# Performance work log

Measured on AMD Instinct MI355X. Metric: run time of the kernel, lower is better.

Reference implementation:

```python
import jax, jax.numpy as jnp
import numpy as np

SIM_RATIO = 0.5
TAU = 1e-4


def _gumbel_softmax_hard(logits, u, axis=-1):
    # torch F.gumbel_softmax(hard=True): straight-through one-hot
    eps = 1e-7
    g = -jnp.log(-jnp.log(u * (1.0 - 2.0 * eps) + eps))
    y_soft = jax.nn.softmax((logits + g) / TAU, axis=axis)
    idx = jnp.argmax(y_soft, axis=axis)
    y_hard = jax.nn.one_hot(idx, logits.shape[axis], dtype=y_soft.dtype)
    return y_hard - jax.lax.stop_gradient(y_soft) + y_soft


def setup_inputs() -> dict:
    key = jax.random.key(0)
    ks = jax.random.split(key, 7)
    N, S, n_items, n_users, d = 4096, 500, 100000, 50000, 64
    need_replace = jax.random.randint(ks[0], (N, 2), 0, n_users)  # user<n_users, item<n_users<=n_items ok
    union_feature = jax.random.normal(ks[1], (N, 2 * d), dtype=jnp.float32)
    all_items = jax.random.normal(ks[2], (n_items, d), dtype=jnp.float32)
    sample_items = jax.random.randint(ks[3], (n_users, S), 0, n_items)
    W = jax.random.normal(ks[4], (d, 2 * d), dtype=jnp.float32) * (1.0 / np.sqrt(2 * d))
    b = jax.random.normal(ks[5], (d,), dtype=jnp.float32) * 0.01
    gumbel_u = jax.random.uniform(ks[6], (N, S), dtype=jnp.float32)
    return {"need_replace": need_replace, "union_feature": union_feature,
            "all_items": all_items, "sample_items": sample_items,
            "W": W, "b": b, "gumbel_u": gumbel_u}


def reference(need_replace, union_feature, all_items, sample_items, W, b, gumbel_u):
    S = sample_items.shape[1]
    user_ids = need_replace[:, 0]
    item_ids = need_replace[:, 1]

    items_emb = all_items[item_ids][:, None, :]          # [N,1,d]
    samp = sample_items[user_ids]                        # [N,S]
    samp_feat = all_items[samp]                          # [N,S,d]

    rank_score = jnp.sum(items_emb * samp_feat, axis=-1)         # [N,S]
    item_ranking = jnp.argsort(rank_score, axis=1)               # ascending sort indices
    item_reverse = jnp.argsort(item_ranking, axis=1)             # rank of each candidate
    sample_item_sort = jnp.take_along_axis(samp, item_ranking, axis=1)  # [N,S]

    uif = union_feature @ W.T + b                                # [N,d]
    replace_score = jnp.sum(uif[:, None, :] * samp_feat, axis=-1)  # [N,S]

    rp = _gumbel_softmax_hard(replace_score, gumbel_u)           # [N,S] one-hot (ST)

    position_index = jnp.sum(item_reverse.astype(rp.dtype) * rp, axis=-1) + 1.0
    similarity = position_index / S
    # MarginLoss (assumed): mean absolute deviation from target ratio
    similarity_loss = jnp.mean(jnp.abs(similarity - SIM_RATIO))

    replaceable_items = jnp.sum(sample_item_sort.astype(rp.dtype) * rp, axis=-1).astype(jnp.int32)
    replaceable_items_feature = jnp.sum(samp_feat * rp[:, :, None], axis=1)  # [N,d]

    return replaceable_items, replaceable_items_feature, similarity_loss, jnp.mean(similarity)
```

## Files before the change

kernel.cpp:

```cpp
#include <hip/hip_runtime.h>

#define SDIM 500
#define DDIM 64
#define NT   256

__device__ __forceinline__ unsigned ford(float x) {
    unsigned u = __float_as_uint(x);
    return u ^ ((unsigned)((int)u >> 31) | 0x80000000u);
}

__device__ __forceinline__ float dot16(float4 a0, float4 a1, float4 a2, float4 a3,
                                       float4 b0, float4 b1, float4 b2, float4 b3) {
    return a0.x*b0.x + a0.y*b0.y + a0.z*b0.z + a0.w*b0.w
         + a1.x*b1.x + a1.y*b1.y + a1.z*b1.z + a1.w*b1.w
         + a2.x*b2.x + a2.y*b2.y + a2.z*b2.z + a2.w*b2.w
         + a3.x*b3.x + a3.y*b3.y + a3.z*b3.z + a3.w*b3.w;
}

__global__ __launch_bounds__(NT) void rs_main(
    const int* __restrict__ need_replace,
    const float* __restrict__ union_feature,
    const float* __restrict__ all_items,
    const int* __restrict__ sample_items,
    const float* __restrict__ Wm,
    const float* __restrict__ bv,
    const float* __restrict__ gumbel_u,
    float* __restrict__ out_items,
    float* __restrict__ out_feat,
    float* __restrict__ ws_sim)
{
    __shared__ __align__(16) float s_uf[128];
    __shared__ __align__(16) float s_uif[DDIM];
    __shared__ unsigned s_fv[SDIM];
    __shared__ float    s_key[SDIM];
    __shared__ int      s_samp[SDIM];
    __shared__ int      s_hist[256];
    __shared__ float    s_mv[4];
    __shared__ int      s_mi[4];
    __shared__ int      s_cnt4[4];
    __shared__ int      s_selb, s_selk, s_k, s_tn;
    __shared__ int      s_tbuf[64];

    const int n    = blockIdx.x;
    const int tid  = threadIdx.x;
    const int wid  = tid >> 6;
    const int part = tid & 3, quad = tid >> 2;

    const int user = need_replace[2 * n];
    const int item = need_replace[2 * n + 1];
    const int*   samp_row = sample_items + (long)user * SDIM;
    const float* gur      = gumbel_u + (long)n * SDIM;

    if (tid < 128) s_uf[tid] = union_feature[(long)n * 128 + tid];
    for (int s = tid; s < SDIM; s += NT) s_samp[s] = samp_row[s];
    const float4* ir = (const float4*)(all_items + (long)item * DDIM) + part * 4;
    const float4 wiA = ir[0], wiB = ir[1], wiC = ir[2], wiD = ir[3];
    __syncthreads();

    {
        const float4* wr4 = (const float4*)(Wm + (long)quad * 128);
        const float4* uf4 = (const float4*)s_uf;
        float acc = 0.f;
        #pragma unroll
        for (int q = 0; q < 8; ++q) {
            float4 w4 = wr4[part + q * 4];
            float4 u4 = uf4[part + q * 4];
            acc += w4.x * u4.x + w4.y * u4.y + w4.z * u4.z + w4.w * u4.w;
        }
        acc += __shfl_xor(acc, 1);
        acc += __shfl_xor(acc, 2);
        if (part == 0) s_uif[quad] = acc + bv[quad];
    }
    __syncthreads();
    const float4* ur = (const float4*)s_uif + part * 4;
    const float4 wuA = ur[0], wuB = ur[1], wuC = ur[2], wuD = ur[3];

    float4 f0, f1, f2, f3;
    {
        const float4* p = (const float4*)(all_items + (long)s_samp[quad] * DDIM) + part * 4;
        f0 = p[0]; f1 = p[1]; f2 = p[2]; f3 = p[3];
    }
    #pragma unroll
    for (int i = 0; i < 8; ++i) {
        const int s = i * 64 + quad;
        float4 g0 = f0, g1 = f1, g2 = f2, g3 = f3;
        if (i < 7) {
            const int sn = s + 64;
            const bool actn = (sn < SDIM);
            const int idxn = s_samp[actn ? sn : 0];
            const float4* q = (const float4*)(all_items + (long)idxn * DDIM) + part * 4;
            if (actn) { g0 = q[0]; g1 = q[1]; g2 = q[2]; g3 = q[3]; }
        }
        const bool act = (s < SDIM);
        float a0 = dot16(f0, f1, f2, f3, wiA, wiB, wiC, wiD);
        float a1 = dot16(f0, f1, f2, f3, wuA, wuB, wuC, wuD);
        a0 += __shfl_xor(a0, 1); a0 += __shfl_xor(a0, 2);
        a1 += __shfl_xor(a1, 1); a1 += __shfl_xor(a1, 2);
        if (act && part == 0) { s_fv[s] = ford(a0); s_key[s] = a1; }
        f0 = g0; f1 = g1; f2 = g2; f3 = g3;
    }
    __syncthreads();

    {
        float bvv = -__builtin_inff();
        int   bii = SDIM;
        for (int s = tid; s < SDIM; s += NT) {
            float u = gur[s];
            float g = -logf(-logf(u * (1.0f - 2e-7f) + 1e-7f));
            float v = s_key[s] + g;
            if (v > bvv) { bvv = v; bii = s; }
        }
        #pragma unroll
        for (int off = 1; off < 64; off <<= 1) {
            float v2 = __shfl_xor(bvv, off); int i2 = __shfl_xor(bii, off);
            if (v2 > bvv || (v2 == bvv && i2 < bii)) { bvv = v2; bii = i2; }
        }
        if ((tid & 63) == 0) { s_mv[wid] = bvv; s_mi[wid] = bii; }
        __syncthreads();
        if (tid == 0) {
            float mv = s_mv[0]; int mi = s_mi[0];
            #pragma unroll
            for (int w = 1; w < 4; ++w) {
                float v2 = s_mv[w]; int i2 = s_mi[w];
                if (v2 > mv || (v2 == mv && i2 < mi)) { mv = v2; mi = i2; }
            }
            s_k = mi;
        }
        __syncthreads();
    }
    const int k = s_k;

    {
        const int src = s_samp[k];
        if (tid < DDIM)
            out_feat[(long)n * DDIM + tid] = all_items[(long)src * DDIM + tid];
    }

    int rank_k;
    {
        const unsigned fvk = s_fv[k];
        int cnt = 0;
        for (int s = tid; s < SDIM; s += NT) {
            unsigned v = s_fv[s];
            cnt += (int)((v < fvk) | ((v == fvk) & (s < k)));
        }
        #pragma unroll
        for (int off = 1; off < 64; off <<= 1) cnt += __shfl_xor(cnt, off);
        if ((tid & 63) == 0) s_cnt4[wid] = cnt;
        __syncthreads();
        rank_k = s_cnt4[0] + s_cnt4[1] + s_cnt4[2] + s_cnt4[3];
    }

    unsigned prefix = 0;
    int krem = k;
    for (int pass = 0; pass < 4; ++pass) {
        const int shift = 24 - 8 * pass;
        s_hist[tid] = 0;
        __syncthreads();
        const unsigned himask = pass ? (0xFFFFFFFFu << (shift + 8)) : 0u;
        for (int s = tid; s < SDIM; s += NT) {
            unsigned v = s_fv[s];
            if ((v & himask) == prefix) atomicAdd(&s_hist[(v >> shift) & 0xFF], 1);
        }
        __syncthreads();
        if (tid < 64) {
            int h0 = s_hist[4*tid], h1 = s_hist[4*tid+1], h2 = s_hist[4*tid+2], h3 = s_hist[4*tid+3];
            int s4 = h0 + h1 + h2 + h3, inc = s4;
            #pragma unroll
            for (int off = 1; off < 64; off <<= 1) {
                int t = __shfl_up(inc, off);
                if (tid >= off) inc += t;
            }
            int base = inc - s4;
            if (krem >= base && krem < inc) {
                if      (krem < base + h0)           { s_selb = 4*tid;   s_selk = krem - base; }
                else if (krem < base + h0 + h1)      { s_selb = 4*tid+1; s_selk = krem - base - h0; }
                else if (krem < base + h0 + h1 + h2) { s_selb = 4*tid+2; s_selk = krem - base - h0 - h1; }
                else                                 { s_selb = 4*tid+3; s_selk = krem - base - h0 - h1 - h2; }
            }
        }
        __syncthreads();
        prefix |= ((unsigned)s_selb) << shift;
        krem = s_selk;
        if (pass == 0) { if (tid == 0) s_tn = 0; }
    }

    __syncthreads();
    for (int s = tid; s < SDIM; s += NT) {
        if (s_fv[s] == prefix) {
            int slot = atomicAdd(&s_tn, 1);
            if (slot < 64) s_tbuf[slot] = s;
        }
    }
    __syncthreads();
    if (tid == 0) {
        int ntie = s_tn;
        int js = s_tbuf[0];
        if (ntie > 1) {
            for (int a = 0; a < ntie; ++a) {
                int c = s_tbuf[a], r = 0;
                for (int b2 = 0; b2 < ntie; ++b2) r += (int)(s_tbuf[b2] < c);
                if (r == krem) js = c;
            }
        }
        out_items[n] = (float)s_samp[js];
        ws_sim[n]    = (float)(rank_k + 1) / (float)SDIM;
    }
}

__global__ __launch_bounds__(NT) void rs_reduce(
    const float* __restrict__ ws_sim, float* __restrict__ out_scal, int N)
{
    __shared__ float s0[NT], s1[NT];
    int tid = threadIdx.x;
    float a = 0.f, m = 0.f;
    for (int i = tid; i < N; i += NT) {
        float sim = ws_sim[i];
        a += fabsf(sim - 0.5f);
        m += sim;
    }
    s0[tid] = a; s1[tid] = m;
    __syncthreads();
    for (int off = NT / 2; off > 0; off >>= 1) {
        if (tid < off) { s0[tid] += s0[tid + off]; s1[tid] += s1[tid + off]; }
        __syncthreads();
    }
    if (tid == 0) {
        out_scal[0] = s0[0] / (float)N;
        out_scal[1] = s1[0] / (float)N;
    }
}

extern "C" void kernel_launch(void* const* d_in, const int* in_sizes, int n_in,
                              void* d_out, int out_size, void* d_ws, size_t ws_size,
                              hipStream_t stream) {
    const int*   need_replace  = (const int*)d_in[0];
    const float* union_feature = (const float*)d_in[1];
    const float* all_items     = (const float*)d_in[2];
    const int*   sample_items  = (const int*)d_in[3];
    const float* Wm            = (const float*)d_in[4];
    const float* bv            = (const float*)d_in[5];
    const float* gumbel_u      = (const float*)d_in[6];

    const int N = in_sizes[0] / 2;

    float* out       = (float*)d_out;
    float* out_items = out;
    float* out_feat  = out + N;
    float* out_scal  = out + N + (long)N * DDIM;
    float* ws_sim    = (float*)d_ws;

    rs_main<<<N, NT, 0, stream>>>(need_replace, union_feature, all_items,
                                  sample_items, Wm, bv, gumbel_u,
                                  out_items, out_feat, ws_sim);
    rs_reduce<<<1, NT, 0, stream>>>(ws_sim, out_scal, N);
}
```

Measured before the change: 81.51 us.

## Split monolithic kernel into separate scoring and selection kernels via workspace

Splits the single per-row kernel into two. rs_score gathers the embeddings and computes both dot-product score arrays, then writes them to workspace. rs_select reads them back and runs the Gumbel argmax, the rank count and the radix select. The aim is a smaller register and shared-memory footprint per kernel, giving higher occupancy for the memory-bound gather phase. The cost is an extra launch and a round trip of about 16 MB through global memory, and the old monolithic path is kept as a fallback when the workspace is too small.

```diff
diff --git a/kernel.cpp b/kernel.cpp
--- a/kernel.cpp
+++ b/kernel.cpp
@@ -3,6 +3,7 @@
 #define SDIM 500
 #define DDIM 64
 #define NT   256
+#define RSTRIDE 512
 
 __device__ __forceinline__ unsigned ford(float x) {
     unsigned u = __float_as_uint(x);
@@ -17,7 +18,232 @@
          + a3.x*b3.x + a3.y*b3.y + a3.z*b3.z + a3.w*b3.w;
 }
 
-__global__ __launch_bounds__(NT) void rs_main(
+__global__ __launch_bounds__(NT) void rs_score(
+    const int* __restrict__ need_replace,
+    const float* __restrict__ union_feature,
+    const float* __restrict__ all_items,
+    const int* __restrict__ sample_items,
+    const float* __restrict__ Wm,
+    const float* __restrict__ bv,
+    unsigned* __restrict__ ws_fv,
+    float* __restrict__ ws_key)
+{
+    __shared__ __align__(16) float s_uf[128];
+    __shared__ __align__(16) float s_uif[DDIM];
+    __shared__ unsigned s_fv[SDIM];
+    __shared__ float    s_key[SDIM];
+    __shared__ int      s_samp[SDIM];
+
+    const int n    = blockIdx.x;
+    const int tid  = threadIdx.x;
+    const int part = tid & 3, quad = tid >> 2;
+
+    const int user = need_replace[2 * n];
+    const int item = need_replace[2 * n + 1];
+    const int* samp_row = sample_items + (long)user * SDIM;
+
+    if (tid < 128) s_uf[tid] = union_feature[(long)n * 128 + tid];
+    for (int s = tid; s < SDIM; s += NT) s_samp[s] = samp_row[s];
+    const float4* ir = (const float4*)(all_items + (long)item * DDIM) + part * 4;
+    const float4 wiA = ir[0], wiB = ir[1], wiC = ir[2], wiD = ir[3];
+    __syncthreads();
+
+    {
+        const float4* wr4 = (const float4*)(Wm + (long)quad * 128);
+        const float4* uf4 = (const float4*)s_uf;
+        float acc = 0.f;
+        #pragma unroll
+        for (int q = 0; q < 8; ++q) {
+            float4 w4 = wr4[part + q * 4];
+            float4 u4 = uf4[part + q * 4];
+            acc += w4.x * u4.x + w4.y * u4.y + w4.z * u4.z + w4.w * u4.w;
+        }
+        acc += __shfl_xor(acc, 1);
+        acc += __shfl_xor(acc, 2);
+        if (part == 0) s_uif[quad] = acc + bv[quad];
+    }
+    __syncthreads();
+    const float4* ur = (const float4*)s_uif + part * 4;
+    const float4 wuA = ur[0], wuB = ur[1], wuC = ur[2], wuD = ur[3];
+
+    float4 f0, f1, f2, f3;
+    {
+        const float4* p = (const float4*)(all_items + (long)s_samp[quad] * DDIM) + part * 4;
+        f0 = p[0]; f1 = p[1]; f2 = p[2]; f3 = p[3];
+    }
+    #pragma unroll
+    for (int i = 0; i < 8; ++i) {
+        const int s = i * 64 + quad;
+        float4 g0 = f0, g1 = f1, g2 = f2, g3 = f3;
+        if (i < 7) {
+            const int sn = s + 64;
+            const bool actn = (sn < SDIM);
+            const int idxn = s_samp[actn ? sn : 0];
+            const float4* q = (const float4*)(all_items + (long)idxn * DDIM) + part * 4;
+            if (actn) { g0 = q[0]; g1 = q[1]; g2 = q[2]; g3 = q[3]; }
+        }
+        const bool act = (s < SDIM);
+        float a0 = dot16(f0, f1, f2, f3, wiA, wiB, wiC, wiD);
+        float a1 = dot16(f0, f1, f2, f3, wuA, wuB, wuC, wuD);
+        a0 += __shfl_xor(a0, 1); a0 += __shfl_xor(a0, 2);
+        a1 += __shfl_xor(a1, 1); a1 += __shfl_xor(a1, 2);
+        if (act && part == 0) { s_fv[s] = ford(a0); s_key[s] = a1; }
+        f0 = g0; f1 = g1; f2 = g2; f3 = g3;
+    }
+    __syncthreads();
+
+    const long rb = (long)n * RSTRIDE;
+    for (int s = tid; s < SDIM; s += NT) {
+        ws_fv[rb + s]  = s_fv[s];
+        ws_key[rb + s] = s_key[s];
+    }
+}
+
+__global__ __launch_bounds__(NT) void rs_select(
+    const int* __restrict__ need_replace,
+    const float* __restrict__ all_items,
+    const int* __restrict__ sample_items,
+    const float* __restrict__ gumbel_u,
+    const unsigned* __restrict__ ws_fv,
+    const float* __restrict__ ws_key,
+    float* __restrict__ out_items,
+    float* __restrict__ out_feat,
+    float* __restrict__ ws_sim)
+{
+    __shared__ unsigned s_fv[SDIM];
+    __shared__ float    s_key[SDIM];
+    __shared__ int      s_samp[SDIM];
+    __shared__ int      s_hist[256];
+    __shared__ float    s_mv[4];
+    __shared__ int      s_mi[4];
+    __shared__ int      s_cnt4[4];
+    __shared__ int      s_selb, s_selk, s_k, s_tn;
+    __shared__ int      s_tbuf[64];
+
+    const int n    = blockIdx.x;
+    const int tid  = threadIdx.x;
+    const int wid  = tid >> 6;
+
+    const int user = need_replace[2 * n];
+    const int* samp_row = sample_items + (long)user * SDIM;
+    const float* gur = gumbel_u + (long)n * SDIM;
+    const long rb = (long)n * RSTRIDE;
+
+    for (int s = tid; s < SDIM; s += NT) {
+        s_fv[s]   = ws_fv[rb + s];
+        s_key[s]  = ws_key[rb + s];
+        s_samp[s] = samp_row[s];
+    }
+    __syncthreads();
+
+    {
+        float bvv = -__builtin_inff();
+        int   bii = SDIM;
+        for (int s = tid; s < SDIM; s += NT) {
+            float u = gur[s];
+            float g = -logf(-logf(u * (1.0f - 2e-7f) + 1e-7f));
+            float v = s_key[s] + g;
+            if (v > bvv) { bvv = v; bii = s; }
+        }
+        #pragma unroll
+        for (int off = 1; off < 64; off <<= 1) {
+            float v2 = __shfl_xor(bvv, off); int i2 = __shfl_xor(bii, off);
+            if (v2 > bvv || (v2 == bvv && i2 < bii)) { bvv = v2; bii = i2; }
+        }
+        if ((tid & 63) == 0) { s_mv[wid] = bvv; s_mi[wid] = bii; }
+        __syncthreads();
+        if (tid == 0) {
+            float mv = s_mv[0]; int mi = s_mi[0];
+            #pragma unroll
+            for (int w = 1; w < 4; ++w) {
+                float v2 = s_mv[w]; int i2 = s_mi[w];
+                if (v2 > mv || (v2 == mv && i2 < mi)) { mv = v2; mi = i2; }
+            }
+            s_k = mi;
+        }
+        __syncthreads();
+    }
+    const int k = s_k;
+
+    {
+        const int src = s_samp[k];
+        if (tid < DDIM)
+            out_feat[(long)n * DDIM + tid] = all_items[(long)src * DDIM + tid];
+    }
+
+    int rank_k;
+    {
+        const unsigned fvk = s_fv[k];
+        int cnt = 0;
+        for (int s = tid; s < SDIM; s += NT) {
+            unsigned v = s_fv[s];
+            cnt += (int)((v < fvk) | ((v == fvk) & (s < k)));
+        }
+        #pragma unroll
+        for (int off = 1; off < 64; off <<= 1) cnt += __shfl_xor(cnt, off);
+        if ((tid & 63) == 0) s_cnt4[wid] = cnt;
+        __syncthreads();
+        rank_k = s_cnt4[0] + s_cnt4[1] + s_cnt4[2] + s_cnt4[3];
+    }
+
+    unsigned prefix = 0;
+    int krem = k;
+    for (int pass = 0; pass < 4; ++pass) {
+        const int shift = 24 - 8 * pass;
+        s_hist[tid] = 0;
+        __syncthreads();
+        const unsigned himask = pass ? (0xFFFFFFFFu << (shift + 8)) : 0u;
+        for (int s = tid; s < SDIM; s += NT) {
+            unsigned v = s_fv[s];
+            if ((v & himask) == prefix) atomicAdd(&s_hist[(v >> shift) & 0xFF], 1);
+        }
+        __syncthreads();
+        if (tid < 64) {
+            int h0 = s_hist[4*tid], h1 = s_hist[4*tid+1], h2 = s_hist[4*tid+2], h3 = s_hist[4*tid+3];
+            int s4 = h0 + h1 + h2 + h3, inc = s4;
+            #pragma unroll
+            for (int off = 1; off < 64; off <<= 1) {
+                int t = __shfl_up(inc, off);
+                if (tid >= off) inc += t;
+            }
+            int base = inc - s4;
+            if (krem >= base && krem < inc) {
+                if      (krem < base + h0)           { s_selb = 4*tid;   s_selk = krem - base; }
+                else if (krem < base + h0 + h1)      { s_selb = 4*tid+1; s_selk = krem - base - h0; }
+                else if (krem < base + h0 + h1 + h2) { s_selb = 4*tid+2; s_selk = krem - base - h0 - h1; }
+                else                                 { s_selb = 4*tid+3; s_selk = krem - base - h0 - h1 - h2; }
+            }
+        }
+        __syncthreads();
+        prefix |= ((unsigned)s_selb) << shift;
+        krem = s_selk;
+        if (pass == 0) { if (tid == 0) s_tn = 0; }
+    }
+
+    __syncthreads();
+    for (int s = tid; s < SDIM; s += NT) {
+        if (s_fv[s] == prefix) {
+            int slot = atomicAdd(&s_tn, 1);
+            if (slot < 64) s_tbuf[slot] = s;
+        }
+    }
+    __syncthreads();
+    if (tid == 0) {
+        int ntie = s_tn;
+        int js = s_tbuf[0];
+        if (ntie > 1) {
+            for (int a = 0; a < ntie; ++a) {
+                int c = s_tbuf[a], r = 0;
+                for (int b2 = 0; b2 < ntie; ++b2) r += (int)(s_tbuf[b2] < c);
+                if (r == krem) js = c;
+            }
+        }
+        out_items[n] = (float)s_samp[js];
+        ws_sim[n]    = (float)(rank_k + 1) / (float)SDIM;
+    }
+}
+
+__global__ __launch_bounds__(NT) void rs_mono(
     const int* __restrict__ need_replace,
     const float* __restrict__ union_feature,
     const float* __restrict__ all_items,
@@ -248,10 +474,26 @@
     float* out_items = out;
     float* out_feat  = out + N;
     float* out_scal  = out + N + (long)N * DDIM;
-    float* ws_sim    = (float*)d_ws;
-
-    rs_main<<<N, NT, 0, stream>>>(need_replace, union_feature, all_items,
-                                  sample_items, Wm, bv, gumbel_u,
-                                  out_items, out_feat, ws_sim);
-    rs_reduce<<<1, NT, 0, stream>>>(ws_sim, out_scal, N);
-}
+
+    const size_t fv_bytes  = (size_t)N * RSTRIDE * sizeof(unsigned);
+    const size_t key_bytes = (size_t)N * RSTRIDE * sizeof(float);
+    const size_t need      = fv_bytes + key_bytes + (size_t)N * sizeof(float);
+
+    if (ws_size >= need) {
+        unsigned* ws_fv  = (unsigned*)d_ws;
+        float*    ws_key = (float*)((char*)d_ws + fv_bytes);
+        float*    ws_sim = (float*)((char*)d_ws + fv_bytes + key_bytes);
+        rs_score<<<N, NT, 0, stream>>>(need_replace, union_feature, all_items,
+                                       sample_items, Wm, bv, ws_fv, ws_key);
+        rs_select<<<N, NT, 0, stream>>>(need_replace, all_items, sample_items,
+                                        gumbel_u, ws_fv, ws_key,
+                                        out_items, out_feat, ws_sim);
+        rs_reduce<<<1, NT, 0, stream>>>(ws_sim, out_scal, N);
+    } else {
+        float* ws_sim = (float*)d_ws;
+        rs_mono<<<N, NT, 0, stream>>>(need_replace, union_feature, all_items,
+                                      sample_items, Wm, bv, gumbel_u,
+                                      out_items, out_feat, ws_sim);
+        rs_reduce<<<1, NT, 0, stream>>>(ws_sim, out_scal, N);
+    }
+}
```

New measurement: 96.89 us. 18.9% more time.
